# Optimization experiments

Measured on AMD Instinct MI355X. Metric: run time of the kernel, lower is better.

## Reference

```python
import jax, jax.numpy as jnp
import numpy as np

D_MODEL = 1024
D_HIDDEN = 4096
NUM_EXPERTS = 8
B, T = 2, 2048


def setup_inputs() -> dict:
    key = jax.random.key(0)
    ks = jax.random.split(key, 8)
    s = 0.02
    x = jax.random.normal(ks[0], (B, T, D_MODEL), dtype=jnp.float32)
    Wg = jax.random.normal(ks[1], (D_MODEL, NUM_EXPERTS), dtype=jnp.float32) * s
    bg = jnp.zeros((NUM_EXPERTS,), dtype=jnp.float32)
    W1 = jax.random.normal(ks[2], (NUM_EXPERTS, D_MODEL, D_HIDDEN), dtype=jnp.float32) * s
    b1 = jnp.zeros((NUM_EXPERTS, D_HIDDEN), dtype=jnp.float32)
    W2 = jax.random.normal(ks[3], (NUM_EXPERTS, D_HIDDEN, D_MODEL), dtype=jnp.float32) * s
    b2 = jnp.zeros((NUM_EXPERTS, D_MODEL), dtype=jnp.float32)
    return {"x": x, "Wg": Wg, "bg": bg, "W1": W1, "b1": b1, "W2": W2, "b2": b2}


def reference(x, Wg, bg, W1, b1, W2, b2):
    # Gating: top-1 routing
    gate_logits = jnp.einsum('btd,de->bte', x, Wg) + bg          # (B,T,E)
    gate_scores = jax.nn.softmax(gate_logits, axis=-1)
    top1_idx = jnp.argmax(gate_scores, axis=-1)                   # (B,T)
    top1_mask = jax.nn.one_hot(top1_idx, NUM_EXPERTS, dtype=x.dtype)  # (B,T,E)
    top1_weight = jnp.sum(gate_scores * top1_mask, axis=-1, keepdims=True)  # (B,T,1)

    # Dense all-expert compute (faithful to the naive original), then mask.
    # For unselected tokens the original computes expert(0)*0 = 0, identical
    # to expert(x)*0 = 0 here.
    h = jax.nn.silu(jnp.einsum('btd,edh->bteh', x, W1) + b1)      # (B,T,E,H)
    o = jnp.einsum('bteh,ehd->bted', h, W2) + b2                  # (B,T,E,D)
    y = jnp.sum(o * top1_mask[..., None], axis=2) * top1_weight   # (B,T,D)
    return y
```

## Files before the change

kernel.cpp:

```cpp
#include <hip/hip_runtime.h>
#include <stdint.h>

#define D_MODEL 1024
#define D_HIDDEN 4096
#define NUM_EXPERTS 8
#define NTOK 4096
#define MAXSLOT 40

typedef __bf16 bf16x8 __attribute__((ext_vector_type(8)));
typedef float floatx4 __attribute__((ext_vector_type(4)));
typedef unsigned int uint2e __attribute__((ext_vector_type(2)));
typedef unsigned int uint4e __attribute__((ext_vector_type(4)));

static __device__ __forceinline__ unsigned short f2bf(float f) {
    union { float f; unsigned int i; } v;
    v.f = f;
    unsigned int i = v.i;
    unsigned int r = (i + 0x7fffu + ((i >> 16) & 1u)) >> 16;
    return (unsigned short)r;
}

static __device__ __forceinline__ void gl_lds16(const unsigned short* g, unsigned short* l) {
    __builtin_amdgcn_global_load_lds(
        (const __attribute__((address_space(1))) void*)g,
        (__attribute__((address_space(3))) void*)l, 16, 0, 0);
}

#define TRRD(dst, addr, off)                                   \
    asm volatile("ds_read_b64_tr_b16 %0, %1 offset:" #off      \
                 : "=v"(dst) : "v"(addr) : "memory")

static __device__ __forceinline__ bf16x8 pack_tr(uint2e a, uint2e b) {
    uint4e p; p.x = a.x; p.y = a.y; p.z = b.x; p.w = b.y;
    return __builtin_bit_cast(bf16x8, p);
}

__global__ __launch_bounds__(256) void convgate_kernel(
    const float* __restrict__ x,
    const float* __restrict__ Wg,
    const float* __restrict__ bg,
    const float* __restrict__ W1,
    const float* __restrict__ W2,
    int* __restrict__ counts,
    int* __restrict__ tlist,
    float* __restrict__ wgt,
    unsigned short* __restrict__ xb,
    unsigned short* __restrict__ w1c,
    unsigned short* __restrict__ w2c)
{
    const int tid = threadIdx.x;
    if (blockIdx.x < 2048) {
        const int bid = blockIdx.x;
        const float* src = (bid < 1024) ? W1 : W2;
        unsigned short* dst = (bid < 1024) ? w1c : w2c;
        const size_t base = (size_t)(bid & 1023) * 32768 + (size_t)tid * 8;
#pragma unroll
        for (int i = 0; i < 16; i++) {
            size_t idx = base + (size_t)i * 2048;
            float4 v0 = *(const float4*)(src + idx);
            float4 v1 = *(const float4*)(src + idx + 4);
            uint4 o;
            o.x = (unsigned)f2bf(v0.x) | ((unsigned)f2bf(v0.y) << 16);
            o.y = (unsigned)f2bf(v0.z) | ((unsigned)f2bf(v0.w) << 16);
            o.z = (unsigned)f2bf(v1.x) | ((unsigned)f2bf(v1.y) << 16);
            o.w = (unsigned)f2bf(v1.z) | ((unsigned)f2bf(v1.w) << 16);
            *(uint4*)(dst + idx) = o;
        }
        return;
    }

    const int wave = tid >> 6;
    const int lane = tid & 63;
    const int tok = (blockIdx.x - 2048) * 4 + wave;

    float acc[NUM_EXPERTS];
#pragma unroll
    for (int e = 0; e < NUM_EXPERTS; e++) acc[e] = 0.f;

    const float4* xr = (const float4*)(x + (size_t)tok * D_MODEL);
    unsigned int* xbr = (unsigned int*)(xb + (size_t)tok * D_MODEL);

#pragma unroll
    for (int i = 0; i < 4; i++) {
        int d4 = i * 64 + lane;
        float4 v = xr[d4];
        unsigned int p0 = (unsigned int)f2bf(v.x) | ((unsigned int)f2bf(v.y) << 16);
        unsigned int p1 = (unsigned int)f2bf(v.z) | ((unsigned int)f2bf(v.w) << 16);
        uint2 pk; pk.x = p0; pk.y = p1;
        *(uint2*)&xbr[d4 * 2] = pk;

        float vc[4] = {v.x, v.y, v.z, v.w};
#pragma unroll
        for (int c = 0; c < 4; c++) {
            const float4* wr = (const float4*)(Wg + (size_t)(d4 * 4 + c) * NUM_EXPERTS);
            float4 w0 = wr[0], w1 = wr[1];
            acc[0] += vc[c] * w0.x; acc[1] += vc[c] * w0.y;
            acc[2] += vc[c] * w0.z; acc[3] += vc[c] * w0.w;
            acc[4] += vc[c] * w1.x; acc[5] += vc[c] * w1.y;
            acc[6] += vc[c] * w1.z; acc[7] += vc[c] * w1.w;
        }
    }
#pragma unroll
    for (int e = 0; e < NUM_EXPERTS; e++) {
        float v = acc[e];
#pragma unroll
        for (int off = 32; off > 0; off >>= 1) v += __shfl_xor(v, off, 64);
        acc[e] = v;
    }
    if (lane == 0) {
        float lg[NUM_EXPERTS];
#pragma unroll
        for (int e = 0; e < NUM_EXPERTS; e++) lg[e] = acc[e] + bg[e];
        int amax = 0;
        float m = lg[0];
#pragma unroll
        for (int e = 1; e < NUM_EXPERTS; e++) {
            if (lg[e] > m) { m = lg[e]; amax = e; }
        }
        float s = 0.f;
#pragma unroll
        for (int e = 0; e < NUM_EXPERTS; e++) s += __expf(lg[e] - m);
        wgt[tok] = 1.0f / s;
        int pos = atomicAdd(&counts[amax], 1);
        tlist[amax * NTOK + pos] = tok;
    }
}

__device__ __forceinline__ bool slot_to_expert(const int* counts, int slot,
                                               int& e_out, int& mt_out, int& cnt_out) {
    int cum = 0;
    for (int i = 0; i < NUM_EXPERTS; i++) {
        int c = counts[i];
        int tt = (c + 127) >> 7;
        if (slot < cum + tt) {
            e_out = i; mt_out = slot - cum; cnt_out = c;
            return true;
        }
        cum += tt;
    }
    return false;
}

__global__ __launch_bounds__(256) void ffn1_kernel(
    const unsigned short* __restrict__ xb,
    const unsigned short* __restrict__ w1c,
    const float* __restrict__ b1,
    const int* __restrict__ counts,
    const int* __restrict__ tlist,
    unsigned short* __restrict__ h)
{
    int e, mt, cnt;
    if (!slot_to_expert(counts, blockIdx.y, e, mt, cnt)) return;
    const int n0 = blockIdx.x * 128;

    __shared__ __align__(16) unsigned short As[2][4096];
    __shared__ __align__(16) unsigned short Bs[2][4096];
    __shared__ int toks[128];

    const int tid = threadIdx.x;
    if (tid < 128) {
        int r = mt * 128 + tid;
        toks[tid] = (r < cnt) ? tlist[e * NTOK + r] : -1;
    }
    __syncthreads();

    const int wave = tid >> 6, lane = tid & 63;
    const int quad = lane >> 4, lm = lane & 15;
    const int mo = (wave & 1) * 64, no = (wave >> 1) * 64;

    const int srow = wave * 16 + (lane >> 2);
    const int kq = (lane & 3) ^ ((lane >> 3) & 3);
    int tA0 = toks[srow], tA1 = toks[64 + srow];
    const unsigned short* a0p = xb + (size_t)(tA0 < 0 ? 0 : tA0) * D_MODEL + kq * 8;
    const unsigned short* a1p = xb + (size_t)(tA1 < 0 ? 0 : tA1) * D_MODEL + kq * 8;

    const unsigned short* w1e = w1c + (size_t)e * D_MODEL * D_HIDDEN;
    const unsigned short* bsrc = w1e + (size_t)(lane >> 1) * D_HIDDEN + n0 + (lane & 1) * 8;

    const int fq = (quad ^ ((lm >> 1) & 3)) * 8;

    const unsigned trb = ((unsigned)(lane >> 4) << 8) | ((unsigned)(lane & 15) << 3);
    const unsigned adB0 = (unsigned)(uintptr_t)&Bs[0][0] + (unsigned)((wave >> 1) * 4096) + trb;
    const unsigned adB1 = (unsigned)(uintptr_t)&Bs[1][0] + (unsigned)((wave >> 1) * 4096) + trb;

    floatx4 acc[4][4];
#pragma unroll
    for (int i = 0; i < 4; i++)
#pragma unroll
        for (int j = 0; j < 4; j++) acc[i][j] = (floatx4){0.f, 0.f, 0.f, 0.f};

#define FFN1_STAGE(b, k0)                                          \
    do {                                                           \
        gl_lds16(a0p + (k0), As[b] + wave * 512);                  \
        gl_lds16(a1p + (k0), As[b] + 2048 + wave * 512);           \
        const unsigned short* bs_ = bsrc + (size_t)(k0) * D_HIDDEN;\
        gl_lds16(bs_ + wave * 16, Bs[b] + wave * 512);             \
        gl_lds16(bs_ + (wave + 4) * 16, Bs[b] + 2048 + wave * 512);\
    } while (0)

#define FFN1_COMPUTE(b, adB)                                                  \
    do {                                                                      \
        bf16x8 af[4];                                                         \
        _Pragma("unroll")                                                     \
        for (int i = 0; i < 4; i++)                                           \
            af[i] = *(const bf16x8*)(As[b] + (mo + i * 16 + lm) * 32 + fq);   \
        uint2e t0, t1, t2, t3, t4, t5, t6, t7;                                \
        TRRD(t0, adB, 0);    TRRD(t1, adB, 128);                              \
        TRRD(t2, adB, 1024); TRRD(t3, adB, 1152);                             \
        TRRD(t4, adB, 2048); TRRD(t5, adB, 2176);                             \
        TRRD(t6, adB, 3072); TRRD(t7, adB, 3200);                             \
        asm volatile("s_waitcnt lgkmcnt(0)" ::: "memory");                    \
        __builtin_amdgcn_sched_barrier(0);                                    \
        bf16x8 bfr[4];                                                        \
        bfr[0] = pack_tr(t0, t1); bfr[1] = pack_tr(t2, t3);                   \
        bfr[2] = pack_tr(t4, t5); bfr[3] = pack_tr(t6, t7);                   \
        _Pragma("unroll")                                                     \
        for (int mi = 0; mi < 4; mi++)                                        \
            _Pragma("unroll")                                                 \
            for (int ni = 0; ni < 4; ni++)                                    \
                acc[mi][ni] = __builtin_amdgcn_mfma_f32_16x16x32_bf16(        \
                    af[mi], bfr[ni], acc[mi][ni], 0, 0, 0);                   \
    } while (0)

    FFN1_STAGE(0, 0);
    __syncthreads();
    int cur = 0;
    for (int k0 = 32; k0 < D_MODEL; k0 += 32) {
        FFN1_STAGE(cur ^ 1, k0);
        unsigned adB = cur ? adB1 : adB0;
        FFN1_COMPUTE(cur, adB);
        __syncthreads();
        cur ^= 1;
    }
    {
        unsigned adB = cur ? adB1 : adB0;
        FFN1_COMPUTE(cur, adB);
    }

    const float* b1e = b1 + (size_t)e * D_HIDDEN;
#pragma unroll
    for (int ni = 0; ni < 4; ni++) {
        int n = n0 + no + ni * 16 + lm;
        float bias = b1e[n];
#pragma unroll
        for (int mi = 0; mi < 4; mi++)
#pragma unroll
            for (int r = 0; r < 4; r++) {
                int m = mo + mi * 16 + quad * 4 + r;
                int tk = toks[m];
                if (tk >= 0) {
                    float z = acc[mi][ni][r] + bias;
                    h[(size_t)tk * D_HIDDEN + n] = f2bf(z / (1.f + __expf(-z)));
                }
            }
    }
}

__global__ __launch_bounds__(256) void ffn2_kernel(
    const unsigned short* __restrict__ h,
    const unsigned short* __restrict__ w2c,
    const float* __restrict__ b2,
    const int* __restrict__ counts,
    const int* __restrict__ tlist,
    const float* __restrict__ wgt,
    float* __restrict__ out)
{
    int e, mt, cnt;
    if (!slot_to_expert(counts, blockIdx.y, e, mt, cnt)) return;
    const int n0 = blockIdx.x * 64;

    __shared__ __align__(16) unsigned short As[2][4096];
    __shared__ __align__(16) unsigned short Bs[2][2048];
    __shared__ int toks[128];

    const int tid = threadIdx.x;
    if (tid < 128) {
        int r = mt * 128 + tid;
        toks[tid] = (r < cnt) ? tlist[e * NTOK + r] : -1;
    }
    __syncthreads();

    const int wave = tid >> 6, lane = tid & 63;
    const int quad = lane >> 4, lm = lane & 15;
    const int mo = (wave & 1) * 64, no = (wave >> 1) * 32;

    const int srow = wave * 16 + (lane >> 2);
    const int kq = (lane & 3) ^ ((lane >> 3) & 3);
    int tA0 = toks[srow], tA1 = toks[64 + srow];
    const unsigned short* a0p = h + (size_t)(tA0 < 0 ? 0 : tA0) * D_HIDDEN + kq * 8;
    const unsigned short* a1p = h + (size_t)(tA1 < 0 ? 0 : tA1) * D_HIDDEN + kq * 8;

    const unsigned short* w2e = w2c + (size_t)e * D_MODEL * D_HIDDEN;
    const unsigned short* bsrc = w2e + (size_t)(lane >> 1) * D_MODEL + n0 + (lane & 1) * 8;

    const int fq = (quad ^ ((lm >> 1) & 3)) * 8;

    const unsigned trb = ((unsigned)(lane >> 4) << 8) | ((unsigned)(lane & 15) << 3);
    const unsigned adB0 = (unsigned)(uintptr_t)&Bs[0][0] + (unsigned)((wave >> 1) * 2048) + trb;
    const unsigned adB1 = (unsigned)(uintptr_t)&Bs[1][0] + (unsigned)((wave >> 1) * 2048) + trb;

    floatx4 acc[4][2];
#pragma unroll
    for (int i = 0; i < 4; i++)
#pragma unroll
        for (int j = 0; j < 2; j++) acc[i][j] = (floatx4){0.f, 0.f, 0.f, 0.f};

#define FFN2_STAGE(b, k0)                                          \
    do {                                                           \
        gl_lds16(a0p + (k0), As[b] + wave * 512);                  \
        gl_lds16(a1p + (k0), As[b] + 2048 + wave * 512);           \
        gl_lds16(bsrc + (size_t)(k0) * D_MODEL + wave * 16,        \
                 Bs[b] + wave * 512);                              \
    } while (0)

#define FFN2_COMPUTE(b, adB)                                                  \
    do {                                                                      \
        bf16x8 af[4];                                                         \
        _Pragma("unroll")                                                     \
        for (int i = 0; i < 4; i++)                                           \
            af[i] = *(const bf16x8*)(As[b] + (mo + i * 16 + lm) * 32 + fq);   \
        uint2e t0, t1, t2, t3;                                                \
        TRRD(t0, adB, 0);    TRRD(t1, adB, 128);                              \
        TRRD(t2, adB, 1024); TRRD(t3, adB, 1152);                             \
        asm volatile("s_waitcnt lgkmcnt(0)" ::: "memory");                    \
        __builtin_amdgcn_sched_barrier(0);                                    \
        bf16x8 bfr[2];                                                        \
        bfr[0] = pack_tr(t0, t1); bfr[1] = pack_tr(t2, t3);                   \
        _Pragma("unroll")                                                     \
        for (int mi = 0; mi < 4; mi++)                                        \
            _Pragma("unroll")                                                 \
            for (int ni = 0; ni < 2; ni++)                                    \
                acc[mi][ni] = __builtin_amdgcn_mfma_f32_16x16x32_bf16(        \
                    af[mi], bfr[ni], acc[mi][ni], 0, 0, 0);                   \
    } while (0)

    FFN2_STAGE(0, 0);
    __syncthreads();
    int cur = 0;
    for (int k0 = 32; k0 < D_HIDDEN; k0 += 32) {
        FFN2_STAGE(cur ^ 1, k0);
        unsigned adB = cur ? adB1 : adB0;
        FFN2_COMPUTE(cur, adB);
        __syncthreads();
        cur ^= 1;
    }
    {
        unsigned adB = cur ? adB1 : adB0;
        FFN2_COMPUTE(cur, adB);
    }

    const float* b2e = b2 + (size_t)e * D_MODEL;
#pragma unroll
    for (int ni = 0; ni < 2; ni++) {
        int n = n0 + no + ni * 16 + lm;
        float bias = b2e[n];
#pragma unroll
        for (int mi = 0; mi < 4; mi++)
#pragma unroll
            for (int r = 0; r < 4; r++) {
                int m = mo + mi * 16 + quad * 4 + r;
                int tk = toks[m];
                if (tk >= 0) {
                    out[(size_t)tk * D_MODEL + n] = (acc[mi][ni][r] + bias) * wgt[tk];
                }
            }
    }
}

extern "C" void kernel_launch(void* const* d_in, const int* in_sizes, int n_in,
                              void* d_out, int out_size, void* d_ws, size_t ws_size,
                              hipStream_t stream) {
    const float* x  = (const float*)d_in[0];
    const float* Wg = (const float*)d_in[1];
    const float* bg = (const float*)d_in[2];
    const float* W1 = (const float*)d_in[3];
    const float* b1 = (const float*)d_in[4];
    const float* W2 = (const float*)d_in[5];
    const float* b2 = (const float*)d_in[6];
    float* out = (float*)d_out;

    char* ws = (char*)d_ws;
    int*   counts = (int*)ws;
    float* wgt    = (float*)(ws + 1024);
    int*   tlist  = (int*)(ws + 32768);
    unsigned short* xb   = (unsigned short*)(ws + 262144);
    unsigned short* hbuf = (unsigned short*)(ws + 8650752);
    unsigned short* w1c  = (unsigned short*)(ws + 42205184);
    unsigned short* w2c  = (unsigned short*)(ws + 109314048);

    hipMemsetAsync(counts, 0, NUM_EXPERTS * sizeof(int), stream);

    convgate_kernel<<<3072, 256, 0, stream>>>(x, Wg, bg, W1, W2,
                                              counts, tlist, wgt, xb, w1c, w2c);
    ffn1_kernel<<<dim3(D_HIDDEN / 128, MAXSLOT), 256, 0, stream>>>(
        xb, w1c, b1, counts, tlist, hbuf);
    ffn2_kernel<<<dim3(D_MODEL / 64, MAXSLOT), 256, 0, stream>>>(
        hbuf, w2c, b2, counts, tlist, wgt, out);
}
```

Before: 573.1 us.

## Enlarge FFN GEMM tiles to 256x256/128x128 with BK=64 and restructure weight conversion

FFN1 now uses 512-thread blocks computing 256x256 output tiles and FFN2 uses 128x128 tiles, both with a K-step of 64 and an XOR swizzle on the A tile. The aim is more reuse per byte loaded into LDS, fewer barriers per K, and better MFMA density. The weight conversion kernel is regridded so each thread loads four strided chunks before converting them, which raises memory-level parallelism. The larger tiles raise register and LDS pressure, which can lower occupancy. FFN1 also has fewer slots (24), so load balance across experts changes.

```diff
diff --git a/kernel.cpp b/kernel.cpp
--- a/kernel.cpp
+++ b/kernel.cpp
@@ -5,7 +5,8 @@
 #define D_HIDDEN 4096
 #define NUM_EXPERTS 8
 #define NTOK 4096
-#define MAXSLOT 40
+#define MAXSLOT1 24
+#define MAXSLOT2 40
 
 typedef __bf16 bf16x8 __attribute__((ext_vector_type(8)));
 typedef float floatx4 __attribute__((ext_vector_type(4)));
@@ -49,29 +50,33 @@
     unsigned short* __restrict__ w2c)
 {
     const int tid = threadIdx.x;
-    if (blockIdx.x < 2048) {
-        const int bid = blockIdx.x;
-        const float* src = (bid < 1024) ? W1 : W2;
-        unsigned short* dst = (bid < 1024) ? w1c : w2c;
-        const size_t base = (size_t)(bid & 1023) * 32768 + (size_t)tid * 8;
-#pragma unroll
-        for (int i = 0; i < 16; i++) {
-            size_t idx = base + (size_t)i * 2048;
-            float4 v0 = *(const float4*)(src + idx);
-            float4 v1 = *(const float4*)(src + idx + 4);
+    if (blockIdx.x < 8192) {
+        const int half = blockIdx.x >> 12;
+        const float* src = half ? W2 : W1;
+        unsigned short* dst = half ? w2c : w1c;
+        const size_t c0 = ((size_t)(blockIdx.x & 4095) * 256 + tid) * 8;
+        float4 v[8];
+#pragma unroll
+        for (int q = 0; q < 4; ++q) {
+            const float* s = src + c0 + (size_t)q * 8388608;
+            v[q * 2]     = *(const float4*)(s);
+            v[q * 2 + 1] = *(const float4*)(s + 4);
+        }
+#pragma unroll
+        for (int q = 0; q < 4; ++q) {
             uint4 o;
-            o.x = (unsigned)f2bf(v0.x) | ((unsigned)f2bf(v0.y) << 16);
-            o.y = (unsigned)f2bf(v0.z) | ((unsigned)f2bf(v0.w) << 16);
-            o.z = (unsigned)f2bf(v1.x) | ((unsigned)f2bf(v1.y) << 16);
-            o.w = (unsigned)f2bf(v1.z) | ((unsigned)f2bf(v1.w) << 16);
-            *(uint4*)(dst + idx) = o;
+            o.x = (unsigned)f2bf(v[q*2].x)   | ((unsigned)f2bf(v[q*2].y) << 16);
+            o.y = (unsigned)f2bf(v[q*2].z)   | ((unsigned)f2bf(v[q*2].w) << 16);
+            o.z = (unsigned)f2bf(v[q*2+1].x) | ((unsigned)f2bf(v[q*2+1].y) << 16);
+            o.w = (unsigned)f2bf(v[q*2+1].z) | ((unsigned)f2bf(v[q*2+1].w) << 16);
+            *(uint4*)(dst + c0 + (size_t)q * 8388608) = o;
         }
         return;
     }
 
     const int wave = tid >> 6;
     const int lane = tid & 63;
-    const int tok = (blockIdx.x - 2048) * 4 + wave;
+    const int tok = (blockIdx.x - 8192) * 4 + wave;
 
     float acc[NUM_EXPERTS];
 #pragma unroll
@@ -126,12 +131,12 @@
     }
 }
 
-__device__ __forceinline__ bool slot_to_expert(const int* counts, int slot,
+__device__ __forceinline__ bool slot_to_expert(const int* counts, int slot, int shift,
                                                int& e_out, int& mt_out, int& cnt_out) {
     int cum = 0;
     for (int i = 0; i < NUM_EXPERTS; i++) {
         int c = counts[i];
-        int tt = (c + 127) >> 7;
+        int tt = (c + (1 << shift) - 1) >> shift;
         if (slot < cum + tt) {
             e_out = i; mt_out = slot - cum; cnt_out = c;
             return true;
@@ -141,7 +146,7 @@
     return false;
 }
 
-__global__ __launch_bounds__(256) void ffn1_kernel(
+__global__ __launch_bounds__(512, 2) void ffn1_kernel(
     const unsigned short* __restrict__ xb,
     const unsigned short* __restrict__ w1c,
     const float* __restrict__ b1,
@@ -150,102 +155,113 @@
     unsigned short* __restrict__ h)
 {
     int e, mt, cnt;
-    if (!slot_to_expert(counts, blockIdx.y, e, mt, cnt)) return;
-    const int n0 = blockIdx.x * 128;
-
-    __shared__ __align__(16) unsigned short As[2][4096];
-    __shared__ __align__(16) unsigned short Bs[2][4096];
-    __shared__ int toks[128];
+    if (!slot_to_expert(counts, blockIdx.y, 8, e, mt, cnt)) return;
+    const int n0 = blockIdx.x * 256;
+
+    __shared__ __align__(16) unsigned short Al[2][256 * 64];
+    __shared__ __align__(16) unsigned short Bl[2][256 * 64];
+    __shared__ int toks[256];
 
     const int tid = threadIdx.x;
-    if (tid < 128) {
-        int r = mt * 128 + tid;
+    if (tid < 256) {
+        int r = mt * 256 + tid;
         toks[tid] = (r < cnt) ? tlist[e * NTOK + r] : -1;
     }
     __syncthreads();
 
     const int wave = tid >> 6, lane = tid & 63;
     const int quad = lane >> 4, lm = lane & 15;
-    const int mo = (wave & 1) * 64, no = (wave >> 1) * 64;
-
-    const int srow = wave * 16 + (lane >> 2);
-    const int kq = (lane & 3) ^ ((lane >> 3) & 3);
-    int tA0 = toks[srow], tA1 = toks[64 + srow];
-    const unsigned short* a0p = xb + (size_t)(tA0 < 0 ? 0 : tA0) * D_MODEL + kq * 8;
-    const unsigned short* a1p = xb + (size_t)(tA1 < 0 ? 0 : tA1) * D_MODEL + kq * 8;
+    const int mo = (wave >> 2) * 128, wc = wave & 3;
+    const int no = wc * 64;
 
     const unsigned short* w1e = w1c + (size_t)e * D_MODEL * D_HIDDEN;
-    const unsigned short* bsrc = w1e + (size_t)(lane >> 1) * D_HIDDEN + n0 + (lane & 1) * 8;
-
-    const int fq = (quad ^ ((lm >> 1) & 3)) * 8;
-
-    const unsigned trb = ((unsigned)(lane >> 4) << 8) | ((unsigned)(lane & 15) << 3);
-    const unsigned adB0 = (unsigned)(uintptr_t)&Bs[0][0] + (unsigned)((wave >> 1) * 4096) + trb;
-    const unsigned adB1 = (unsigned)(uintptr_t)&Bs[1][0] + (unsigned)((wave >> 1) * 4096) + trb;
-
-    floatx4 acc[4][4];
-#pragma unroll
-    for (int i = 0; i < 4; i++)
+    const int ag = ((tid & 7) ^ ((tid >> 3) & 7)) * 8;
+    const unsigned short* asrc[4];
+#pragma unroll
+    for (int j = 0; j < 4; ++j) {
+        int m = j * 64 + (tid >> 3);
+        int tk = toks[m];
+        asrc[j] = xb + (size_t)(tk < 0 ? 0 : tk) * D_MODEL + ag;
+    }
+    const int bk = (tid >> 1) & 63, bn8 = (tid & 1) * 8;
+    const unsigned short* bsrc[4];
+#pragma unroll
+    for (int j = 0; j < 4; ++j) {
+        int nb = j * 4 + (tid >> 7);
+        bsrc[j] = w1e + (size_t)bk * D_HIDDEN + n0 + nb * 16 + bn8;
+    }
+
+#define F1_STAGE(p, k0)                                                  \
+    do {                                                                 \
+        _Pragma("unroll")                                                \
+        for (int j = 0; j < 4; ++j)                                      \
+            gl_lds16(asrc[j] + (k0), &Al[p][j * 4096 + wave * 512]);     \
+        _Pragma("unroll")                                                \
+        for (int j = 0; j < 4; ++j)                                      \
+            gl_lds16(bsrc[j] + (size_t)(k0) * D_HIDDEN,                  \
+                     &Bl[p][j * 4096 + wave * 512]);                     \
+    } while (0)
+
+#define F1_COMPUTE(p)                                                         \
+    do {                                                                      \
+        const unsigned short* Ab = &Al[p][0];                                 \
+        const unsigned bvB = (unsigned)(uintptr_t)&Bl[p][0]                   \
+                           + (unsigned)(wc * 8192 + quad * 256 + lm * 8);     \
+        _Pragma("unroll")                                                     \
+        for (int s = 0; s < 2; ++s) {                                         \
+            bf16x8 af[8];                                                     \
+            const int gsw = ((s * 4 + quad) ^ (lm & 7)) * 8;                  \
+            _Pragma("unroll")                                                 \
+            for (int i = 0; i < 8; ++i)                                       \
+                af[i] = *(const bf16x8*)(Ab + (mo + i * 16 + lm) * 64 + gsw); \
+            uint2e t0, t1, t2, t3, t4, t5, t6, t7;                            \
+            const unsigned vs = bvB + s * 1024;                               \
+            unsigned v0 = vs, v1 = vs + 2048, v2 = vs + 4096, v3 = vs + 6144; \
+            TRRD(t0, v0, 0); TRRD(t1, v0, 128);                               \
+            TRRD(t2, v1, 0); TRRD(t3, v1, 128);                               \
+            TRRD(t4, v2, 0); TRRD(t5, v2, 128);                               \
+            TRRD(t6, v3, 0); TRRD(t7, v3, 128);                               \
+            asm volatile("s_waitcnt lgkmcnt(0)" ::: "memory");                \
+            __builtin_amdgcn_sched_barrier(0);                                \
+            bf16x8 bf[4];                                                     \
+            bf[0] = pack_tr(t0, t1); bf[1] = pack_tr(t2, t3);                 \
+            bf[2] = pack_tr(t4, t5); bf[3] = pack_tr(t6, t7);                 \
+            _Pragma("unroll")                                                 \
+            for (int i = 0; i < 8; ++i)                                       \
+                _Pragma("unroll")                                             \
+                for (int j = 0; j < 4; ++j)                                   \
+                    acc[i][j] = __builtin_amdgcn_mfma_f32_16x16x32_bf16(      \
+                        af[i], bf[j], acc[i][j], 0, 0, 0);                    \
+        }                                                                     \
+    } while (0)
+
+    floatx4 acc[8][4];
+#pragma unroll
+    for (int i = 0; i < 8; i++)
 #pragma unroll
         for (int j = 0; j < 4; j++) acc[i][j] = (floatx4){0.f, 0.f, 0.f, 0.f};
 
-#define FFN1_STAGE(b, k0)                                          \
-    do {                                                           \
-        gl_lds16(a0p + (k0), As[b] + wave * 512);                  \
-        gl_lds16(a1p + (k0), As[b] + 2048 + wave * 512);           \
-        const unsigned short* bs_ = bsrc + (size_t)(k0) * D_HIDDEN;\
-        gl_lds16(bs_ + wave * 16, Bs[b] + wave * 512);             \
-        gl_lds16(bs_ + (wave + 4) * 16, Bs[b] + 2048 + wave * 512);\
-    } while (0)
-
-#define FFN1_COMPUTE(b, adB)                                                  \
-    do {                                                                      \
-        bf16x8 af[4];                                                         \
-        _Pragma("unroll")                                                     \
-        for (int i = 0; i < 4; i++)                                           \
-            af[i] = *(const bf16x8*)(As[b] + (mo + i * 16 + lm) * 32 + fq);   \
-        uint2e t0, t1, t2, t3, t4, t5, t6, t7;                                \
-        TRRD(t0, adB, 0);    TRRD(t1, adB, 128);                              \
-        TRRD(t2, adB, 1024); TRRD(t3, adB, 1152);                             \
-        TRRD(t4, adB, 2048); TRRD(t5, adB, 2176);                             \
-        TRRD(t6, adB, 3072); TRRD(t7, adB, 3200);                             \
-        asm volatile("s_waitcnt lgkmcnt(0)" ::: "memory");                    \
-        __builtin_amdgcn_sched_barrier(0);                                    \
-        bf16x8 bfr[4];                                                        \
-        bfr[0] = pack_tr(t0, t1); bfr[1] = pack_tr(t2, t3);                   \
-        bfr[2] = pack_tr(t4, t5); bfr[3] = pack_tr(t6, t7);                   \
-        _Pragma("unroll")                                                     \
-        for (int mi = 0; mi < 4; mi++)                                        \
-            _Pragma("unroll")                                                 \
-            for (int ni = 0; ni < 4; ni++)                                    \
-                acc[mi][ni] = __builtin_amdgcn_mfma_f32_16x16x32_bf16(        \
-                    af[mi], bfr[ni], acc[mi][ni], 0, 0, 0);                   \
-    } while (0)
-
-    FFN1_STAGE(0, 0);
+    const int NT = D_MODEL / 64;
+    F1_STAGE(0, 0);
     __syncthreads();
     int cur = 0;
-    for (int k0 = 32; k0 < D_MODEL; k0 += 32) {
-        FFN1_STAGE(cur ^ 1, k0);
-        unsigned adB = cur ? adB1 : adB0;
-        FFN1_COMPUTE(cur, adB);
+    for (int kt = 1; kt < NT; ++kt) {
+        F1_STAGE(cur ^ 1, kt * 64);
+        F1_COMPUTE(cur);
         __syncthreads();
         cur ^= 1;
     }
-    {
-        unsigned adB = cur ? adB1 : adB0;
-        FFN1_COMPUTE(cur, adB);
-    }
+    F1_COMPUTE(cur);
 
     const float* b1e = b1 + (size_t)e * D_HIDDEN;
 #pragma unroll
-    for (int ni = 0; ni < 4; ni++) {
+    for (int ni = 0; ni < 4; ++ni) {
         int n = n0 + no + ni * 16 + lm;
         float bias = b1e[n];
 #pragma unroll
-        for (int mi = 0; mi < 4; mi++)
-#pragma unroll
-            for (int r = 0; r < 4; r++) {
+        for (int mi = 0; mi < 8; ++mi)
+#pragma unroll
+            for (int r = 0; r < 4; ++r) {
                 int m = mo + mi * 16 + quad * 4 + r;
                 int tk = toks[m];
                 if (tk >= 0) {
@@ -256,7 +272,7 @@
     }
 }
 
-__global__ __launch_bounds__(256) void ffn2_kernel(
+__global__ __launch_bounds__(256, 2) void ffn2_kernel(
     const unsigned short* __restrict__ h,
     const unsigned short* __restrict__ w2c,
     const float* __restrict__ b2,
@@ -266,11 +282,11 @@
     float* __restrict__ out)
 {
     int e, mt, cnt;
-    if (!slot_to_expert(counts, blockIdx.y, e, mt, cnt)) return;
-    const int n0 = blockIdx.x * 64;
-
-    __shared__ __align__(16) unsigned short As[2][4096];
-    __shared__ __align__(16) unsigned short Bs[2][2048];
+    if (!slot_to_expert(counts, blockIdx.y, 7, e, mt, cnt)) return;
+    const int n0 = blockIdx.x * 128;
+
+    __shared__ __align__(16) unsigned short Al[2][128 * 64];
+    __shared__ __align__(16) unsigned short Bl[2][128 * 64];
     __shared__ int toks[128];
 
     const int tid = threadIdx.x;
@@ -282,82 +298,97 @@
 
     const int wave = tid >> 6, lane = tid & 63;
     const int quad = lane >> 4, lm = lane & 15;
-    const int mo = (wave & 1) * 64, no = (wave >> 1) * 32;
-
-    const int srow = wave * 16 + (lane >> 2);
-    const int kq = (lane & 3) ^ ((lane >> 3) & 3);
-    int tA0 = toks[srow], tA1 = toks[64 + srow];
-    const unsigned short* a0p = h + (size_t)(tA0 < 0 ? 0 : tA0) * D_HIDDEN + kq * 8;
-    const unsigned short* a1p = h + (size_t)(tA1 < 0 ? 0 : tA1) * D_HIDDEN + kq * 8;
+    const int mo = (wave & 1) * 64, wc = wave >> 1;
+    const int no = wc * 64;
 
     const unsigned short* w2e = w2c + (size_t)e * D_MODEL * D_HIDDEN;
-    const unsigned short* bsrc = w2e + (size_t)(lane >> 1) * D_MODEL + n0 + (lane & 1) * 8;
-
-    const int fq = (quad ^ ((lm >> 1) & 3)) * 8;
-
-    const unsigned trb = ((unsigned)(lane >> 4) << 8) | ((unsigned)(lane & 15) << 3);
-    const unsigned adB0 = (unsigned)(uintptr_t)&Bs[0][0] + (unsigned)((wave >> 1) * 2048) + trb;
-    const unsigned adB1 = (unsigned)(uintptr_t)&Bs[1][0] + (unsigned)((wave >> 1) * 2048) + trb;
-
-    floatx4 acc[4][2];
+    const int ag = ((tid & 7) ^ ((tid >> 3) & 7)) * 8;
+    const unsigned short* asrc[4];
+#pragma unroll
+    for (int j = 0; j < 4; ++j) {
+        int m = j * 32 + (tid >> 3);
+        int tk = toks[m];
+        asrc[j] = h + (size_t)(tk < 0 ? 0 : tk) * D_HIDDEN + ag;
+    }
+    const int bk = (tid >> 1) & 63, bn8 = (tid & 1) * 8;
+    const unsigned short* bsrc[4];
+#pragma unroll
+    for (int j = 0; j < 4; ++j) {
+        int nb = j * 2 + (tid >> 7);
+        bsrc[j] = w2e + (size_t)bk * D_MODEL + n0 + nb * 16 + bn8;
+    }
+
+#define F2_STAGE(p, k0)                                                  \
+    do {                                                                 \
+        _Pragma("unroll")                                                \
+        for (int j = 0; j < 4; ++j)                                      \
+            gl_lds16(asrc[j] + (k0), &Al[p][j * 2048 + wave * 512]);     \
+        _Pragma("unroll")                                                \
+        for (int j = 0; j < 4; ++j)                                      \
+            gl_lds16(bsrc[j] + (size_t)(k0) * D_MODEL,                   \
+                     &Bl[p][j * 2048 + wave * 512]);                     \
+    } while (0)
+
+#define F2_COMPUTE(p)                                                         \
+    do {                                                                      \
+        const unsigned short* Ab = &Al[p][0];                                 \
+        const unsigned bvB = (unsigned)(uintptr_t)&Bl[p][0]                   \
+                           + (unsigned)(wc * 8192 + quad * 256 + lm * 8);     \
+        _Pragma("unroll")                                                     \
+        for (int s = 0; s < 2; ++s) {                                         \
+            bf16x8 af[4];                                                     \
+            const int gsw = ((s * 4 + quad) ^ (lm & 7)) * 8;                  \
+            _Pragma("unroll")                                                 \
+            for (int i = 0; i < 4; ++i)                                       \
+                af[i] = *(const bf16x8*)(Ab + (mo + i * 16 + lm) * 64 + gsw); \
+            uint2e t0, t1, t2, t3, t4, t5, t6, t7;                            \
+            const unsigned vs = bvB + s * 1024;                               \
+            unsigned v0 = vs, v1 = vs + 2048, v2 = vs + 4096, v3 = vs + 6144; \
+            TRRD(t0, v0, 0); TRRD(t1, v0, 128);                               \
+            TRRD(t2, v1, 0); TRRD(t3, v1, 128);                               \
+            TRRD(t4, v2, 0); TRRD(t5, v2, 128);                               \
+            TRRD(t6, v3, 0); TRRD(t7, v3, 128);                               \
+            asm volatile("s_waitcnt lgkmcnt(0)" ::: "memory");                \
+            __builtin_amdgcn_sched_barrier(0);                                \
+            bf16x8 bf[4];                                                     \
+            bf[0] = pack_tr(t0, t1); bf[1] = pack_tr(t2, t3);                 \
+            bf[2] = pack_tr(t4, t5); bf[3] = pack_tr(t6, t7);                 \
+            _Pragma("unroll")                                                 \
+            for (int i = 0; i < 4; ++i)                                       \
+                _Pragma("unroll")                                             \
+                for (int j = 0; j < 4; ++j)                                   \
+                    acc[i][j] = __builtin_amdgcn_mfma_f32_16x16x32_bf16(      \
+                        af[i], bf[j], acc[i][j], 0, 0, 0);                    \
+        }                                                                     \
+    } while (0)
+
+    floatx4 acc[4][4];
 #pragma unroll
     for (int i = 0; i < 4; i++)
 #pragma unroll
-        for (int j = 0; j < 2; j++) acc[i][j] = (floatx4){0.f, 0.f, 0.f, 0.f};
-
-#define FFN2_STAGE(b, k0)                                          \
-    do {                                                           \
-        gl_lds16(a0p + (k0), As[b] + wave * 512);                  \
-        gl_lds16(a1p + (k0), As[b] + 2048 + wave * 512);           \
-        gl_lds16(bsrc + (size_t)(k0) * D_MODEL + wave * 16,        \
-                 Bs[b] + wave * 512);                              \
-    } while (0)
-
-#define FFN2_COMPUTE(b, adB)                                                  \
-    do {                                                                      \
-        bf16x8 af[4];                                                         \
-        _Pragma("unroll")                                                     \
-        for (int i = 0; i < 4; i++)                                           \
-            af[i] = *(const bf16x8*)(As[b] + (mo + i * 16 + lm) * 32 + fq);   \
-        uint2e t0, t1, t2, t3;                                                \
-        TRRD(t0, adB, 0);    TRRD(t1, adB, 128);                              \
-        TRRD(t2, adB, 1024); TRRD(t3, adB, 1152);                             \
-        asm volatile("s_waitcnt lgkmcnt(0)" ::: "memory");                    \
-        __builtin_amdgcn_sched_barrier(0);                                    \
-        bf16x8 bfr[2];                                                        \
-        bfr[0] = pack_tr(t0, t1); bfr[1] = pack_tr(t2, t3);                   \
-        _Pragma("unroll")                                                     \
-        for (int mi = 0; mi < 4; mi++)                                        \
-            _Pragma("unroll")                                                 \
-            for (int ni = 0; ni < 2; ni++)                                    \
-                acc[mi][ni] = __builtin_amdgcn_mfma_f32_16x16x32_bf16(        \
-                    af[mi], bfr[ni], acc[mi][ni], 0, 0, 0);                   \
-    } while (0)
-
-    FFN2_STAGE(0, 0);
+        for (int j = 0; j < 4; j++) acc[i][j] = (floatx4){0.f, 0.f, 0.f, 0.f};
+
+    const int NT = D_HIDDEN / 64;
+    F2_STAGE(0, 0);
     __syncthreads();
     int cur = 0;
-    for (int k0 = 32; k0 < D_HIDDEN; k0 += 32) {
-        FFN2_STAGE(cur ^ 1, k0);
-        unsigned adB = cur ? adB1 : adB0;
-        FFN2_COMPUTE(cur, adB);
+    for (int kt = 1; kt < NT; ++kt) {
+        F2_STAGE(cur ^ 1, kt * 64);
+        F2_COMPUTE(cur);
         __syncthreads();
         cur ^= 1;
     }
-    {
-        unsigned adB = cur ? adB1 : adB0;
-        FFN2_COMPUTE(cur, adB);
-    }
+    F2_COMPUTE(cur);
 
     const float* b2e = b2 + (size_t)e * D_MODEL;
 #pragma unroll
-    for (int ni = 0; ni < 2; ni++) {
+    for (int ni = 0; ni < 4; ++ni) {
         int n = n0 + no + ni * 16 + lm;
         float bias = b2e[n];
 #pragma unroll
-        for (int mi = 0; mi < 4; mi++)
-#pragma unroll
-            for (int r = 0; r < 4; r++) {
+        for (int mi = 0; mi < 4; ++mi)
+#pragma unroll
+            for (int r = 0; r < 4; ++r) {
                 int m = mo + mi * 16 + quad * 4 + r;
                 int tk = toks[m];
                 if (tk >= 0) {
@@ -390,10 +421,10 @@
 
     hipMemsetAsync(counts, 0, NUM_EXPERTS * sizeof(int), stream);
 
-    convgate_kernel<<<3072, 256, 0, stream>>>(x, Wg, bg, W1, W2,
+    convgate_kernel<<<9216, 256, 0, stream>>>(x, Wg, bg, W1, W2,
                                               counts, tlist, wgt, xb, w1c, w2c);
-    ffn1_kernel<<<dim3(D_HIDDEN / 128, MAXSLOT), 256, 0, stream>>>(
+    ffn1_kernel<<<dim3(D_HIDDEN / 256, MAXSLOT1), 512, 0, stream>>>(
         xb, w1c, b1, counts, tlist, hbuf);
-    ffn2_kernel<<<dim3(D_MODEL / 64, MAXSLOT), 256, 0, stream>>>(
+    ffn2_kernel<<<dim3(D_MODEL / 128, MAXSLOT2), 256, 0, stream>>>(
         hbuf, w2c, b2, counts, tlist, wgt, out);
 }
```

Result: no change. 563.8 us (-1.6%).
